# Performance work log

Hardware: AMD Instinct MI355X
Metric: run time of the kernel (lower is better)

Reference implementation:

```python
import jax, jax.numpy as jnp
import numpy as np
from jax import lax

DIM = 256; HEADS = 16; DHEAD = 16; H = 12; W = 26
DS = 4; KOFF = 6; OSCALE = 4.0
SCALE = DHEAD ** -0.5
EPS = 1e-5


def _create_grid(hh, ww, dtype):
    # channel0 = x (width index), channel1 = y (height index); matches torch meshgrid(arange(w), arange(h), indexing='xy')
    gy, gx = jnp.meshgrid(jnp.arange(hh, dtype=dtype), jnp.arange(ww, dtype=dtype), indexing='ij')
    return jnp.stack([gx, gy], axis=0)  # (2, hh, ww)


def _grid_sample_bilinear(img, grid):
    # F.grid_sample, mode='bilinear', padding_mode='zeros', align_corners=False
    # img (B,C,Hi,Wi); grid (B,Ho,Wo,2), grid[...,0]=x-norm, grid[...,1]=y-norm in [-1,1]
    B, C, Hi, Wi = img.shape
    x = ((grid[..., 0] + 1.0) * Wi - 1.0) / 2.0
    y = ((grid[..., 1] + 1.0) * Hi - 1.0) / 2.0
    x0 = jnp.floor(x); y0 = jnp.floor(y)

    def gather(xi, yi):
        valid = ((xi >= 0) & (xi < Wi) & (yi >= 0) & (yi < Hi)).astype(img.dtype)
        xc = jnp.clip(xi, 0, Wi - 1).astype(jnp.int32)
        yc = jnp.clip(yi, 0, Hi - 1).astype(jnp.int32)
        v = jax.vmap(lambda im, yy, xx: im[:, yy, xx])(img, yc, xc)  # (B,C,Ho,Wo)
        return v * valid[:, None]

    wx1 = (x - x0)[:, None]; wx0 = 1.0 - wx1
    wy1 = (y - y0)[:, None]; wy0 = 1.0 - wy1
    return (gather(x0, y0) * wy0 * wx0 + gather(x0 + 1.0, y0) * wy0 * wx1
            + gather(x0, y0 + 1.0) * wy1 * wx0 + gather(x0 + 1.0, y0 + 1.0) * wy1 * wx1)


def _forward(x, q, w_off_dw, b_off_dw, w_off_pw, wk, wv, w_out, b_out,
             cpb_w1, cpb_b1, cpb_w2, cpb_b2, cpb_w3, cpb_b3,
             conv1d_w, conv1d_b, ln_g, ln_b):
    b = x.shape[0]
    # faithful to torch: q.repeat(1,1,h*w).view(bs,1,dim,h,w).squeeze(1) == tile then reshape
    q_map = jnp.tile(q[:, 0, :], (1, H * W)).reshape(b, DIM, H, W)

    # to_offsets: depthwise Conv2d(k=6,s=4,p=1) -> GELU -> 1x1 conv (no bias) -> tanh -> *offset_scale
    t = lax.conv_general_dilated(q_map, w_off_dw, window_strides=(DS, DS),
                                 padding=[(1, 1), (1, 1)], feature_group_count=DIM,
                                 dimension_numbers=('NCHW', 'OIHW', 'NCHW'))
    t = jax.nn.gelu(t + b_off_dw[None, :, None, None], approximate=False)
    off = jnp.tanh(jnp.einsum('oc,bchw->bohw', w_off_pw, t)) * OSCALE  # (b,2,Hk,Wk)
    Hk, Wk = off.shape[-2], off.shape[-1]  # 3, 6

    gkv = _create_grid(Hk, Wk, x.dtype)
    vg0 = gkv[0] + off[:, 0]
    vg1 = gkv[1] + off[:, 1]
    # faithful repo normalize_grid: channel0 / (h-1), channel1 / (w-1)
    n0 = 2.0 * vg0 / max(Hk - 1, 1) - 1.0
    n1 = 2.0 * vg1 / max(Wk - 1, 1) - 1.0
    vgrid_scaled = jnp.stack([n0, n1], axis=-1)  # (b, Hk, Wk, 2)

    kv = _grid_sample_bilinear(x, vgrid_scaled)  # (b, DIM, Hk, Wk)
    k = jnp.einsum('oc,bchw->bohw', wk, kv)
    v = jnp.einsum('oc,bchw->bohw', wv, kv)

    qh = (q_map * SCALE).reshape(b, HEADS, DHEAD, H * W).transpose(0, 1, 3, 2)  # (b,h,i,d)
    kh = k.reshape(b, HEADS, DHEAD, Hk * Wk).transpose(0, 1, 3, 2)              # (b,h,j,d)
    vh = v.reshape(b, HEADS, DHEAD, Hk * Wk).transpose(0, 1, 3, 2)
    sim = jnp.einsum('bhid,bhjd->bhij', qh, kh)  # (b,16,312,18)

    # CPB relative position bias
    gq = _create_grid(H, W, x.dtype)
    gq0 = 2.0 * gq[0] / max(H - 1, 1) - 1.0
    gq1 = 2.0 * gq[1] / max(W - 1, 1) - 1.0
    grid_q = jnp.stack([gq0, gq1], axis=-1).reshape(1, H * W, 2)
    grid_kv = vgrid_scaled.reshape(b, Hk * Wk, 2)
    pos = grid_q[:, :, None, :] - grid_kv[:, None, :, :]       # (b,i,j,2)
    bias = jnp.sign(pos) * jnp.log(jnp.abs(pos) + 1.0)
    bias = jax.nn.relu(bias @ cpb_w1.T + cpb_b1)
    bias = jax.nn.relu(bias @ cpb_w2.T + cpb_b2)
    bias = bias @ cpb_w3.T + cpb_b3                             # (b,i,j,heads)
    sim = sim + bias.transpose(0, 3, 1, 2)

    attn = jax.nn.softmax(sim, axis=-1)  # dropout(0.1) identity in eval
    out = jnp.einsum('bhij,bhjd->bhid', attn, vh)               # (b,h,i,d)
    out = out.transpose(0, 1, 3, 2).reshape(b, DIM, H, W)        # 'b h (x y) d -> b (h d) x y'
    out = jnp.einsum('oc,bchw->bohw', w_out, out) + b_out[None, :, None, None]

    # SpatialCrossAttention tail: view -> permute -> Conv1d(312,1,1) -> residual -> LayerNorm
    tokens = out.reshape(b, DIM, H * W).transpose(0, 2, 1)       # (b,312,256)
    pooled = jnp.einsum('t,btc->bc', conv1d_w, tokens)[:, None, :] + conv1d_b[None, :, None]
    y = pooled + q
    mu = y.mean(-1, keepdims=True)
    var = y.var(-1, keepdims=True)
    return (y - mu) / jnp.sqrt(var + EPS) * ln_g + ln_b          # (b,1,256)


def setup_inputs() -> dict:
    key = jax.random.key(0)
    ks = jax.random.split(key, 16)
    rn = lambda i, shape, s=0.02: jax.random.normal(ks[i], shape, dtype=jnp.float32) * s
    B = 256
    return {
        'x': jax.random.normal(ks[0], (B, DIM, H, W), dtype=jnp.float32),
        'q': jax.random.normal(ks[1], (B, 1, DIM), dtype=jnp.float32),
        'w_off_dw': rn(2, (DIM, 1, KOFF, KOFF), 0.05),
        'b_off_dw': jnp.zeros((DIM,), jnp.float32),
        'w_off_pw': rn(3, (2, DIM), 0.05),
        'wk': rn(4, (DIM, DIM)),
        'wv': rn(5, (DIM, DIM)),
        'w_out': rn(6, (DIM, DIM)),
        'b_out': jnp.zeros((DIM,), jnp.float32),
        'cpb_w1': rn(7, (64, 2), 0.1),
        'cpb_b1': jnp.zeros((64,), jnp.float32),
        'cpb_w2': rn(8, (64, 64), 0.1),
        'cpb_b2': jnp.zeros((64,), jnp.float32),
        'cpb_w3': rn(9, (HEADS, 64), 0.1),
        'cpb_b3': jnp.zeros((HEADS,), jnp.float32),
        'conv1d_w': rn(10, (H * W,), 0.05),
        'conv1d_b': jnp.zeros((1,), jnp.float32),
        'ln_g': jnp.ones((DIM,), jnp.float32),
        'ln_b': jnp.zeros((DIM,), jnp.float32),
    }


def reference(x, q, w_off_dw, b_off_dw, w_off_pw, wk, wv, w_out, b_out,
              cpb_w1, cpb_b1, cpb_w2, cpb_b2, cpb_w3, cpb_b3,
              conv1d_w, conv1d_b, ln_g, ln_b):
    return _forward(x, q, w_off_dw, b_off_dw, w_off_pw, wk, wv, w_out, b_out,
                    cpb_w1, cpb_b1, cpb_w2, cpb_b2, cpb_w3, cpb_b3,
                    conv1d_w, conv1d_b, ln_g, ln_b)
```

## Files before the change

### kernel.cpp

```cpp
#include <hip/hip_runtime.h>
#include <hip/hip_bf16.h>
#include <math.h>


typedef __attribute__((ext_vector_type(8))) short short8;
typedef __attribute__((ext_vector_type(4))) short s4bf;
typedef __attribute__((ext_vector_type(4))) float floatx4;

union U16 { uint4 u; short8 s; };
union U8b { unsigned int u[2]; s4bf s; };

#define MFMA(A, B, C) __builtin_amdgcn_mfma_f32_16x16x32_bf16((A), (B), (C), 0, 0, 0)
#define MFMA16(A, B, C) __builtin_amdgcn_mfma_f32_16x16x16bf16_1k((A), (B), (C), 0, 0, 0)

__device__ __forceinline__ unsigned int f2bf(float f) {
    unsigned int u = __float_as_uint(f);
    u += 0x7fffu + ((u >> 16) & 1u);
    return u >> 16;
}
__device__ __forceinline__ unsigned int pk2(float a, float b) {
    __hip_bfloat162 h = __float22bfloat162_rn(make_float2(a, b));
    union { __hip_bfloat162 h; unsigned int u; } cv; cv.h = h;
    return cv.u;
}
__device__ __forceinline__ float bf2f(unsigned short v) {
    return __uint_as_float((unsigned int)v << 16);
}
__device__ __forceinline__ uint4 pack8(float4 a, float4 b) {
    uint4 r;
    r.x = pk2(a.x, a.y); r.y = pk2(a.z, a.w);
    r.z = pk2(b.x, b.y); r.w = pk2(b.z, b.w);
    return r;
}

__global__ __launch_bounds__(512, 2) void k_all(
    const float* __restrict__ x, const float* __restrict__ q,
    const float* __restrict__ w_dw, const float* __restrict__ b_dw,
    const float* __restrict__ w_pw,
    const float* __restrict__ wk, const float* __restrict__ wv,
    const float* __restrict__ w_out, const float* __restrict__ b_out,
    const float* __restrict__ cw1, const float* __restrict__ cb1,
    const float* __restrict__ cw2, const float* __restrict__ cb2,
    const float* __restrict__ cw3, const float* __restrict__ cb3,
    const float* __restrict__ conv_w, const float* __restrict__ conv_b,
    const float* __restrict__ ln_g, const float* __restrict__ ln_b,
    float* __restrict__ out)
{
    const int b = blockIdx.x, tid = threadIdx.x;
    const int w = tid >> 6, lane = tid & 63;
    const int n = lane & 15, qd = lane >> 4;

    __shared__ float qf_s[256];
    __shared__ unsigned short q_sb[256];
    __shared__ unsigned short v_sb[5120];
    __shared__ float F0[468], F1[216];
    __shared__ unsigned int lutxy[312];
    __shared__ float off_s[36], n0_s[18], n1_s[18];
    __shared__ float sx0[18], sy0[18], swx[18], swy[18];
    __shared__ float b2_s[64], b3_s[16];
    __shared__ __align__(16) float w1p[4][8][8];
    __shared__ float wA_s[288];
    __shared__ __align__(16) float m_s[256];
    __shared__ float pooled_s[256], redb[24];
    __shared__ __align__(16) unsigned char UB[117504];
    float* Sbuf = (float*)UB;
    unsigned short* kvT = (unsigned short*)UB;
    float* qsw = (float*)UB;
    float* t_s = (float*)(UB + 16512);
    unsigned short* k_sb = (unsigned short*)(UB + 16512);
    float* wred = (float*)(UB + 39168);

    if (tid < 256) {
        const float qv = q[b * 256 + tid];
        qf_s[tid] = qv;
        q_sb[tid] = (unsigned short)f2bf(qv * 0.25f);
    }
    for (int u = tid; u < 4128; u += 512) {
        const int r = u / 258, i = u - r * 258;
        qsw[u] = (i < 256) ? q[b * 256 + i] : 0.f;
    }
    if (tid < 312) {
        const int iy = tid / 26;
        lutxy[tid] = (unsigned int)(tid - iy * 26) | ((unsigned int)iy << 16);
    }
    if (tid < 64) b2_s[tid] = cb2[tid];
    if (tid < 16) b3_s[tid] = cb3[tid];
    if (tid >= 64 && tid < 96) {
        const int t2 = tid - 64;
        const int qdi = t2 >> 3, kp = t2 & 7;
        const int kk0 = 2 * kp, kk1 = 2 * kp + 1;
        const int kid0 = (kk0 < 8) ? (qdi * 8 + kk0) : (32 + qdi * 8 + kk0 - 8);
        const int kid1 = (kk1 < 8) ? (qdi * 8 + kk1) : (32 + qdi * 8 + kk1 - 8);
        w1p[qdi][kp][0] = cw1[kid0 * 2];
        w1p[qdi][kp][1] = cw1[kid0 * 2 + 1];
        w1p[qdi][kp][2] = cb1[kid0];
        w1p[qdi][kp][3] = cw1[kid1 * 2];
        w1p[qdi][kp][4] = cw1[kid1 * 2 + 1];
        w1p[qdi][kp][5] = cb1[kid1];
    }
    __syncthreads();

    {
        const int c = tid & 255, g = tid >> 8;
        float wreg[36];
        const float4* wdw4 = (const float4*)w_dw;
        #pragma unroll
        for (int i = 0; i < 9; ++i) {
            const float4 t4 = wdw4[c * 9 + i];
            wreg[i * 4 + 0] = t4.x; wreg[i * 4 + 1] = t4.y;
            wreg[i * 4 + 2] = t4.z; wreg[i * 4 + 3] = t4.w;
        }
        float acc[9];
        const float bv = b_dw[c];
        #pragma unroll
        for (int a = 0; a < 9; ++a) acc[a] = bv;
        const int cb = (c * 56) & 255;
        const int cp = (c & 15) * 258;
        for (int jh = 0; jh < 3; ++jh) {
            for (int kh = 0; kh < 6; ++kh) {
                const int ih = jh * 4 - 1 + kh;
                if (ih < 0 || ih >= 12) continue;
                const int rb = ih * 26;
                #pragma unroll
                for (int jwl = 0; jwl < 3; ++jwl) {
                    const int jw = g * 3 + jwl;
                    #pragma unroll
                    for (int kw = 0; kw < 6; ++kw) {
                        const int iw = jw * 4 - 1 + kw;
                        if (iw < 0 || iw >= 26) continue;
                        acc[jh * 3 + jwl] += wreg[kh * 6 + kw] * qsw[cp + ((cb + rb + iw) & 255)];
                    }
                }
            }
        }
        #pragma unroll
        for (int a = 0; a < 9; ++a) {
            const int jh = a / 3, jwl = a - jh * 3;
            const int p = jh * 6 + g * 3 + jwl;
            const float v = acc[a];
            t_s[p * 256 + c] = 0.5f * v * (1.0f + erff(v * 0.70710678118654752f));
        }
    }
    __syncthreads();

    for (int oi = w; oi < 36; oi += 8) {
        const int o = oi / 18, p = oi - o * 18;
        float s = 0.f;
        for (int c = lane; c < 256; c += 64) s += w_pw[o * 256 + c] * t_s[p * 256 + c];
        for (int d = 32; d > 0; d >>= 1) s += __shfl_down(s, d, 64);
        if (lane == 0) off_s[oi] = 4.0f * tanhf(s);
    }
    __syncthreads();

    if (tid < 18) {
        const int j = tid, jh = j / 6, jw = j - jh * 6;
        const float vg0 = (float)jw + off_s[j];
        const float vg1 = (float)jh + off_s[18 + j];
        const float n0 = 2.0f * vg0 / 2.0f - 1.0f;
        const float n1 = 2.0f * vg1 / 5.0f - 1.0f;
        n0_s[j] = n0; n1_s[j] = n1;
        const float xp = ((n0 + 1.0f) * 26.0f - 1.0f) * 0.5f;
        const float yp = ((n1 + 1.0f) * 12.0f - 1.0f) * 0.5f;
        const float x0 = floorf(xp), y0 = floorf(yp);
        sx0[j] = x0; sy0[j] = y0; swx[j] = xp - x0; swy[j] = yp - y0;
    }
    __syncthreads();

    {
        const int c = tid & 255, g = tid >> 8;
        const float* xb = x + ((size_t)b * 256 + c) * 312;
        for (int jj = 0; jj < 9; ++jj) {
            const int j = g * 9 + jj;
            const int x0 = (int)sx0[j], y0 = (int)sy0[j];
            const int x1 = x0 + 1, y1 = y0 + 1;
            const float wx1 = swx[j], wy1 = swy[j];
            const float wx0 = 1.f - wx1, wy0 = 1.f - wy1;
            const bool xv0 = (x0 >= 0) & (x0 < 26), xv1 = (x1 >= 0) & (x1 < 26);
            const bool yv0 = (y0 >= 0) & (y0 < 12), yv1 = (y1 >= 0) & (y1 < 12);
            const float v00 = (xv0 & yv0) ? xb[y0 * 26 + x0] : 0.f;
            const float v01 = (xv1 & yv0) ? xb[y0 * 26 + x1] : 0.f;
            const float v10 = (xv0 & yv1) ? xb[y1 * 26 + x0] : 0.f;
            const float v11 = (xv1 & yv1) ? xb[y1 * 26 + x1] : 0.f;
            const float val = wy0 * (wx0 * v00 + wx1 * v01) + wy1 * (wx0 * v10 + wx1 * v11);
            kvT[j * 264 + c] = (unsigned short)f2bf(val);
        }
    }
    for (int u = tid; u < 684; u += 512) {
        if (u < 468) {
            const int ixv = u / 18, j = u - ixv * 18;
            const float p0 = (float)ixv * (2.0f / 11.0f) - 1.0f - n0_s[j];
            F0[u] = copysignf(__logf(1.0f + fabsf(p0)), p0);
        } else {
            const int u2 = u - 468;
            const int iyv = u2 / 18, j = u2 - iyv * 18;
            const float p1 = (float)iyv * (2.0f / 25.0f) - 1.0f - n1_s[j];
            F1[u2] = copysignf(__logf(1.0f + fabsf(p1)), p1);
        }
    }
    __syncthreads();

    {
        const int m2 = w & 1, mtb = w >> 1;
        const float4* wm4 = (const float4*)(m2 ? wv : wk);
        floatx4 pa[4][2];
        #pragma unroll
        for (int a = 0; a < 4; ++a) {
            pa[a][0] = (floatx4){0.f, 0.f, 0.f, 0.f};
            pa[a][1] = (floatx4){0.f, 0.f, 0.f, 0.f};
        }
        #pragma unroll 2
        for (int ks = 0; ks < 8; ++ks) {
            U16 b0, b1;
            b0.u = *(const uint4*)(kvT + n * 264 + ks * 32 + qd * 8);
            b1.u = make_uint4(0u, 0u, 0u, 0u);
            if (n < 2) b1.u = *(const uint4*)(kvT + (16 + n) * 264 + ks * 32 + qd * 8);
            #pragma unroll
            for (int mtl = 0; mtl < 4; ++mtl) {
                const int mt = mtb + mtl * 4;
                const int f4i = (mt * 16 + n) * 64 + ks * 8 + qd * 2;
                U16 A; A.u = pack8(wm4[f4i], wm4[f4i + 1]);
                pa[mtl][0] = MFMA(A.s, b0.s, pa[mtl][0]);
                pa[mtl][1] = MFMA(A.s, b1.s, pa[mtl][1]);
            }
        }
        unsigned short* dst = m2 ? v_sb : k_sb;
        #pragma unroll
        for (int mtl = 0; mtl < 4; ++mtl) {
            const int mt = mtb + mtl * 4;
            #pragma unroll
            for (int r = 0; r < 4; ++r) {
                const int o = mt * 16 + qd * 4 + r;
                dst[o * 20 + n] = (unsigned short)f2bf(pa[mtl][0][r]);
                if (n < 2) dst[o * 20 + 16 + n] = (unsigned short)f2bf(pa[mtl][1][r]);
            }
        }
    }
    __syncthreads();

    uint4 W2f[4][2];
    unsigned int W3h[4][2];
    {
        const float4* cw2_4 = (const float4*)cw2;
        #pragma unroll
        for (int mtl = 0; mtl < 4; ++mtl)
            #pragma unroll
            for (int ks = 0; ks < 2; ++ks) {
                const int base = (mtl * 16 + n) * 16 + ks * 8 + qd * 2;
                W2f[mtl][ks] = pack8(cw2_4[base], cw2_4[base + 1]);
            }
        const float4* cw3_4 = (const float4*)cw3;
        #pragma unroll
        for (int kc = 0; kc < 4; ++kc) {
            const float4 v = cw3_4[n * 16 + kc * 4 + qd];
            W3h[kc][0] = pk2(v.x, v.y);
            W3h[kc][1] = pk2(v.z, v.w);
        }
    }

    unsigned int Bk16[2][2][2];
    #pragma unroll
    for (int hh = 0; hh < 2; ++hh)
        #pragma unroll
        for (int jt = 0; jt < 2; ++jt) {
            unsigned int u0 = 0, u1 = 0;
            const int j = jt * 16 + n;
            if (j < 18) {
                const int h = w * 2 + hh;
                const int cb0 = (h * 16 + qd * 4) * 20 + j;
                u0 = (unsigned)k_sb[cb0]      | ((unsigned)k_sb[cb0 + 20] << 16);
                u1 = (unsigned)k_sb[cb0 + 40] | ((unsigned)k_sb[cb0 + 60] << 16);
            }
            Bk16[hh][jt][0] = u0; Bk16[hh][jt][1] = u1;
        }
    int kA[2];
    #pragma unroll
    for (int hh = 0; hh < 2; ++hh)
        kA[hh] = (((w * 2 + hh) * 16 + qd * 4) * 56) & 255;
    __syncthreads();

    float wAcc[18];
    #pragma unroll
    for (int j = 0; j < 18; ++j) wAcc[j] = 0.f;

    auto soft_acc = [&](int chp, const float* Sp) {
        const int il = tid >> 4, h = tid & 15;
        const int CIp = (chp == 9) ? 24 : 32;
        if (il < CIp) {
            const float cwv = conv_w[chp * 32 + il];
            float lv[18];
            const float* row = Sp + (il * 18) * 17 + h;
            #pragma unroll
            for (int j = 0; j < 18; ++j) lv[j] = row[j * 17];
            float mx[9];
            #pragma unroll
            for (int p = 0; p < 9; ++p) mx[p] = fmaxf(lv[2 * p], lv[2 * p + 1]);
            #pragma unroll
            for (int p = 0; p < 4; ++p) mx[p] = fmaxf(mx[p], mx[p + 4]);
            mx[0] = fmaxf(mx[0], mx[2]); mx[1] = fmaxf(mx[1], mx[3]);
            const float m = fmaxf(fmaxf(mx[0], mx[1]), mx[8]);
            float sa = 0.f, sb = 0.f;
            #pragma unroll
            for (int j = 0; j < 18; j += 2) {
                lv[j] = __expf(lv[j] - m);     sa += lv[j];
                lv[j + 1] = __expf(lv[j + 1] - m); sb += lv[j + 1];
            }
            const float wgt = cwv / (sa + sb);
            #pragma unroll
            for (int j = 0; j < 18; ++j) wAcc[j] = fmaf(wgt, lv[j], wAcc[j]);
        }
    };

    for (int t = 0; t < 12; ++t) {
        if (t < 10) {
            float* Sc = Sbuf + (t % 3) * 9792;
            const int ibase = t * 32;
            #pragma unroll
            for (int hh = 0; hh < 2; ++hh) {
                const int h = w * 2 + hh;
                const int ka = kA[hh];
                #pragma unroll
                for (int ig = 0; ig < 2; ++ig) {
                    const int ii = ibase + ig * 16 + n;
                    const unsigned int a0 =
                        (unsigned)q_sb[(ka + ii) & 255] |
                        ((unsigned)q_sb[(ka + 56 + ii) & 255] << 16);
                    const unsigned int a1 =
                        (unsigned)q_sb[(ka + 112 + ii) & 255] |
                        ((unsigned)q_sb[(ka + 168 + ii) & 255] << 16);
                    U8b Af; Af.u[0] = a0; Af.u[1] = a1;
                    #pragma unroll
                    for (int jt = 0; jt < 2; ++jt) {
                        U8b Bf; Bf.u[0] = Bk16[hh][jt][0]; Bf.u[1] = Bk16[hh][jt][1];
                        floatx4 D = {0.f, 0.f, 0.f, 0.f};
                        D = MFMA16(Af.s, Bf.s, D);
                        const int j = jt * 16 + n;
                        if (j < 18) {
                            #pragma unroll
                            for (int r = 0; r < 4; ++r)
                                Sc[((ig * 16 + qd * 4 + r) * 18 + j) * 17 + h] = D[r];
                        }
                    }
                }
            }
        }
        if (t >= 1 && t < 11) {
            const int chm = t - 1;
            float* Sm = Sbuf + (chm % 3) * 9792;
            const int ibase = chm * 32;
            auto mlp1 = [&](int tt) {
                const int ig = (tt >= 18) ? 1 : 0;
                const int j = tt - ig * 18;
                const int i0 = ibase + ig * 16 + n;
                const unsigned int lv2 = lutxy[(i0 < 312) ? i0 : 311];
                const int ix = (int)(lv2 & 0xffffu), iy = (int)(lv2 >> 16);
                const float f0 = F0[ix * 18 + j];
                const float f1 = F1[iy * 18 + j];
                U16 ub0, ub1;
                {
                    unsigned int uu[8];
                    #pragma unroll
                    for (int kp = 0; kp < 8; ++kp) {
                        const float* wp = &w1p[qd][kp][0];
                        const float ha = fmaxf(fmaf(wp[0], f0, fmaf(wp[1], f1, wp[2])), 0.f);
                        const float hb = fmaxf(fmaf(wp[3], f0, fmaf(wp[4], f1, wp[5])), 0.f);
                        uu[kp] = pk2(ha, hb);
                    }
                    ub0.u = make_uint4(uu[0], uu[1], uu[2], uu[3]);
                    ub1.u = make_uint4(uu[4], uu[5], uu[6], uu[7]);
                }
                floatx4 a3a = {0.f, 0.f, 0.f, 0.f};
                floatx4 a3b = {0.f, 0.f, 0.f, 0.f};
                #pragma unroll
                for (int mtl = 0; mtl < 4; ++mtl) {
                    U16 A0, A1; A0.u = W2f[mtl][0]; A1.u = W2f[mtl][1];
                    floatx4 acc = {0.f, 0.f, 0.f, 0.f};
                    acc = MFMA(A0.s, ub0.s, acc);
                    acc = MFMA(A1.s, ub1.s, acc);
                    U8b Bf3, Af3;
                    Bf3.u[0] = pk2(fmaxf(acc[0] + b2_s[mtl*16 + qd*4 + 0], 0.f),
                                   fmaxf(acc[1] + b2_s[mtl*16 + qd*4 + 1], 0.f));
                    Bf3.u[1] = pk2(fmaxf(acc[2] + b2_s[mtl*16 + qd*4 + 2], 0.f),
                                   fmaxf(acc[3] + b2_s[mtl*16 + qd*4 + 3], 0.f));
                    Af3.u[0] = W3h[mtl][0]; Af3.u[1] = W3h[mtl][1];
                    if (mtl & 1) a3b = MFMA16(Af3.s, Bf3.s, a3b);
                    else         a3a = MFMA16(Af3.s, Bf3.s, a3a);
                }
                float* sp = Sm + ((ig * 16 + n) * 18 + j) * 17 + qd * 4;
                #pragma unroll
                for (int r = 0; r < 4; ++r)
                    sp[r] = a3a[r] + a3b[r] + b3_s[qd * 4 + r] + sp[r];
            };
            mlp1(w);
            mlp1(w + 8);
            mlp1(w + 16);
            mlp1(w + 24);
            if (w < 4) mlp1(32 + w);
        }
        if (t >= 2) soft_acc(t - 2, Sbuf + ((t - 2) % 3) * 9792);
        __syncthreads();
    }

    #pragma unroll
    for (int j = 0; j < 18; ++j) wred[tid * 18 + j] = wAcc[j];
    {
        float v = 0.f;
        for (int u = tid; u < 312; u += 512) v += conv_w[u];
        for (int d = 32; d > 0; d >>= 1) v += __shfl_down(v, d, 64);
        if (lane == 0) redb[w] = v;
    }
    __syncthreads();
    for (int u = tid; u < 288; u += 512) {
        const int h = u / 18, j = u - h * 18;
        float s = 0.f;
        #pragma unroll
        for (int sl = 0; sl < 32; ++sl) s += wred[(sl * 16 + h) * 18 + j];
        wA_s[u] = s;
    }
    __syncthreads();

    if (tid < 256) {
        const int hb = (tid >> 4) * 18;
        float acc = 0.f;
        #pragma unroll
        for (int j = 0; j < 18; ++j) acc += wA_s[hb + j] * bf2f(v_sb[tid * 20 + j]);
        m_s[tid] = acc;
    }
    __syncthreads();

    float Ssum = 0.f;
    #pragma unroll
    for (int i = 0; i < 8; ++i) Ssum += redb[i];

    {
        const float4 mm = *(const float4*)(m_s + lane * 4);
        for (int ol = 0; ol < 32; ++ol) {
            const int o = w * 32 + ol;
            const float4 wq = *(const float4*)(w_out + o * 256 + lane * 4);
            float d = wq.x * mm.x + wq.y * mm.y + wq.z * mm.z + wq.w * mm.w;
            for (int dd = 32; dd > 0; dd >>= 1) d += __shfl_down(d, dd, 64);
            if (lane == 0) pooled_s[o] = d;
        }
    }
    __syncthreads();

    if (tid < 256) {
        const float y = pooled_s[tid] + b_out[tid] * Ssum + conv_b[0] + qf_s[tid];
        float s1 = y, s2 = y * y;
        for (int d = 32; d > 0; d >>= 1) { s1 += __shfl_down(s1, d, 64); s2 += __shfl_down(s2, d, 64); }
        if (lane == 0) { redb[16 + w] = s1; redb[20 + w] = s2; }
    }
    __syncthreads();
    if (tid < 256) {
        const float y = pooled_s[tid] + b_out[tid] * Ssum + conv_b[0] + qf_s[tid];
        const float S1 = redb[16] + redb[17] + redb[18] + redb[19];
        const float S2 = redb[20] + redb[21] + redb[22] + redb[23];
        const float mu = S1 * (1.0f / 256.0f);
        const float var = S2 * (1.0f / 256.0f) - mu * mu;
        out[b * 256 + tid] = (y - mu) * rsqrtf(var + 1e-5f) * ln_g[tid] + ln_b[tid];
    }
}

extern "C" void kernel_launch(void* const* d_in, const int* in_sizes, int n_in,
                              void* d_out, int out_size, void* d_ws, size_t ws_size,
                              hipStream_t stream) {
    const float* x       = (const float*)d_in[0];
    const float* q       = (const float*)d_in[1];
    const float* w_dw    = (const float*)d_in[2];
    const float* b_dwp   = (const float*)d_in[3];
    const float* w_pw    = (const float*)d_in[4];
    const float* wk      = (const float*)d_in[5];
    const float* wv      = (const float*)d_in[6];
    const float* w_out   = (const float*)d_in[7];
    const float* b_out   = (const float*)d_in[8];
    const float* cw1     = (const float*)d_in[9];
    const float* cb1     = (const float*)d_in[10];
    const float* cw2     = (const float*)d_in[11];
    const float* cb2     = (const float*)d_in[12];
    const float* cw3     = (const float*)d_in[13];
    const float* cb3     = (const float*)d_in[14];
    const float* conv_w  = (const float*)d_in[15];
    const float* conv_b  = (const float*)d_in[16];
    const float* ln_g    = (const float*)d_in[17];
    const float* ln_b    = (const float*)d_in[18];
    float* out = (float*)d_out;

    k_all<<<256, 512, 0, stream>>>(x, q, w_dw, b_dwp, w_pw, wk, wv, w_out, b_out,
                                   cw1, cb1, cw2, cb2, cw3, cb3,
                                   conv_w, conv_b, ln_g, ln_b, out);
}
```

Baseline: 248.5 us.

## Register-cache CPB layer-1 weights, pair MLP tiles, replicate q buffer per quad

Moves the first CPB MLP layer's weights and biases from shared memory into per-lane registers and processes two (i,j) tiles per call so their MFMA chains interleave. Replicates the bf16 q vector four times in shared memory at a 272-element stride so each lane quad reads its own copy, aiming to cut LDS bank conflicts on the score A-fragment gathers. This adds 48 live floats per thread under launch_bounds(512,2), which risks register spills.

```diff
diff --git a/kernel.cpp b/kernel.cpp
--- a/kernel.cpp
+++ b/kernel.cpp
@@ -51,14 +51,13 @@
     const int n = lane & 15, qd = lane >> 4;
 
     __shared__ float qf_s[256];
-    __shared__ unsigned short q_sb[256];
+    __shared__ unsigned short q_sb4[1088];
     __shared__ unsigned short v_sb[5120];
     __shared__ float F0[468], F1[216];
     __shared__ unsigned int lutxy[312];
     __shared__ float off_s[36], n0_s[18], n1_s[18];
     __shared__ float sx0[18], sy0[18], swx[18], swy[18];
     __shared__ float b2_s[64], b3_s[16];
-    __shared__ __align__(16) float w1p[4][8][8];
     __shared__ float wA_s[288];
     __shared__ __align__(16) float m_s[256];
     __shared__ float pooled_s[256], redb[24];
@@ -73,7 +72,9 @@
     if (tid < 256) {
         const float qv = q[b * 256 + tid];
         qf_s[tid] = qv;
-        q_sb[tid] = (unsigned short)f2bf(qv * 0.25f);
+        const unsigned short qb = (unsigned short)f2bf(qv * 0.25f);
+        q_sb4[tid] = qb; q_sb4[272 + tid] = qb;
+        q_sb4[544 + tid] = qb; q_sb4[816 + tid] = qb;
     }
     for (int u = tid; u < 4128; u += 512) {
         const int r = u / 258, i = u - r * 258;
@@ -85,19 +86,6 @@
     }
     if (tid < 64) b2_s[tid] = cb2[tid];
     if (tid < 16) b3_s[tid] = cb3[tid];
-    if (tid >= 64 && tid < 96) {
-        const int t2 = tid - 64;
-        const int qdi = t2 >> 3, kp = t2 & 7;
-        const int kk0 = 2 * kp, kk1 = 2 * kp + 1;
-        const int kid0 = (kk0 < 8) ? (qdi * 8 + kk0) : (32 + qdi * 8 + kk0 - 8);
-        const int kid1 = (kk1 < 8) ? (qdi * 8 + kk1) : (32 + qdi * 8 + kk1 - 8);
-        w1p[qdi][kp][0] = cw1[kid0 * 2];
-        w1p[qdi][kp][1] = cw1[kid0 * 2 + 1];
-        w1p[qdi][kp][2] = cb1[kid0];
-        w1p[qdi][kp][3] = cw1[kid1 * 2];
-        w1p[qdi][kp][4] = cw1[kid1 * 2 + 1];
-        w1p[qdi][kp][5] = cb1[kid1];
-    }
     __syncthreads();
 
     {
@@ -256,6 +244,12 @@
             W3h[kc][1] = pk2(v.z, v.w);
         }
     }
+    float W1a[16], W1b[16], B1r[16];
+    #pragma unroll
+    for (int kk = 0; kk < 16; ++kk) {
+        const int kid = (kk < 8) ? (qd * 8 + kk) : (32 + qd * 8 + kk - 8);
+        W1a[kk] = cw1[kid * 2]; W1b[kk] = cw1[kid * 2 + 1]; B1r[kk] = cb1[kid];
+    }
 
     unsigned int Bk16[2][2][2];
     #pragma unroll
@@ -314,6 +308,7 @@
         if (t < 10) {
             float* Sc = Sbuf + (t % 3) * 9792;
             const int ibase = t * 32;
+            const unsigned short* qsb = q_sb4 + qd * 272;
             #pragma unroll
             for (int hh = 0; hh < 2; ++hh) {
                 const int h = w * 2 + hh;
@@ -322,11 +317,11 @@
                 for (int ig = 0; ig < 2; ++ig) {
                     const int ii = ibase + ig * 16 + n;
                     const unsigned int a0 =
-                        (unsigned)q_sb[(ka + ii) & 255] |
-                        ((unsigned)q_sb[(ka + 56 + ii) & 255] << 16);
+                        (unsigned)qsb[(ka + ii) & 255] |
+                        ((unsigned)qsb[(ka + 56 + ii) & 255] << 16);
                     const unsigned int a1 =
-                        (unsigned)q_sb[(ka + 112 + ii) & 255] |
-                        ((unsigned)q_sb[(ka + 168 + ii) & 255] << 16);
+                        (unsigned)qsb[(ka + 112 + ii) & 255] |
+                        ((unsigned)qsb[(ka + 168 + ii) & 255] << 16);
                     U8b Af; Af.u[0] = a0; Af.u[1] = a1;
                     #pragma unroll
                     for (int jt = 0; jt < 2; ++jt) {
@@ -347,54 +342,71 @@
             const int chm = t - 1;
             float* Sm = Sbuf + (chm % 3) * 9792;
             const int ibase = chm * 32;
-            auto mlp1 = [&](int tt) {
-                const int ig = (tt >= 18) ? 1 : 0;
-                const int j = tt - ig * 18;
-                const int i0 = ibase + ig * 16 + n;
-                const unsigned int lv2 = lutxy[(i0 < 312) ? i0 : 311];
-                const int ix = (int)(lv2 & 0xffffu), iy = (int)(lv2 >> 16);
-                const float f0 = F0[ix * 18 + j];
-                const float f1 = F1[iy * 18 + j];
-                U16 ub0, ub1;
-                {
+            auto mlp2 = [&](int tA, int tB, bool two) {
+                int igv[2], jv[2];
+                float f0v[2], f1v[2];
+                #pragma unroll
+                for (int u = 0; u < 2; ++u) {
+                    const int tt = u ? tB : tA;
+                    const int ig = (tt >= 18) ? 1 : 0;
+                    const int j = tt - ig * 18;
+                    igv[u] = ig; jv[u] = j;
+                    const int i0 = ibase + ig * 16 + n;
+                    const unsigned int lv2 = lutxy[(i0 < 312) ? i0 : 311];
+                    const int ix = (int)(lv2 & 0xffffu), iy = (int)(lv2 >> 16);
+                    f0v[u] = F0[ix * 18 + j];
+                    f1v[u] = F1[iy * 18 + j];
+                }
+                U16 ub0[2], ub1[2];
+                #pragma unroll
+                for (int u = 0; u < 2; ++u) {
                     unsigned int uu[8];
                     #pragma unroll
                     for (int kp = 0; kp < 8; ++kp) {
-                        const float* wp = &w1p[qd][kp][0];
-                        const float ha = fmaxf(fmaf(wp[0], f0, fmaf(wp[1], f1, wp[2])), 0.f);
-                        const float hb = fmaxf(fmaf(wp[3], f0, fmaf(wp[4], f1, wp[5])), 0.f);
+                        const float ha = fmaxf(fmaf(W1a[2*kp],   f0v[u], fmaf(W1b[2*kp],   f1v[u], B1r[2*kp])),   0.f);
+                        const float hb = fmaxf(fmaf(W1a[2*kp+1], f0v[u], fmaf(W1b[2*kp+1], f1v[u], B1r[2*kp+1])), 0.f);
                         uu[kp] = pk2(ha, hb);
                     }
-                    ub0.u = make_uint4(uu[0], uu[1], uu[2], uu[3]);
-                    ub1.u = make_uint4(uu[4], uu[5], uu[6], uu[7]);
-                }
-                floatx4 a3a = {0.f, 0.f, 0.f, 0.f};
-                floatx4 a3b = {0.f, 0.f, 0.f, 0.f};
+                    ub0[u].u = make_uint4(uu[0], uu[1], uu[2], uu[3]);
+                    ub1[u].u = make_uint4(uu[4], uu[5], uu[6], uu[7]);
+                }
+                floatx4 a3a[2], a3b[2];
+                #pragma unroll
+                for (int u = 0; u < 2; ++u) {
+                    a3a[u] = (floatx4){0.f, 0.f, 0.f, 0.f};
+                    a3b[u] = (floatx4){0.f, 0.f, 0.f, 0.f};
+                }
                 #pragma unroll
                 for (int mtl = 0; mtl < 4; ++mtl) {
                     U16 A0, A1; A0.u = W2f[mtl][0]; A1.u = W2f[mtl][1];
-                    floatx4 acc = {0.f, 0.f, 0.f, 0.f};
-                    acc = MFMA(A0.s, ub0.s, acc);
-                    acc = MFMA(A1.s, ub1.s, acc);
-                    U8b Bf3, Af3;
-                    Bf3.u[0] = pk2(fmaxf(acc[0] + b2_s[mtl*16 + qd*4 + 0], 0.f),
-                                   fmaxf(acc[1] + b2_s[mtl*16 + qd*4 + 1], 0.f));
-                    Bf3.u[1] = pk2(fmaxf(acc[2] + b2_s[mtl*16 + qd*4 + 2], 0.f),
-                                   fmaxf(acc[3] + b2_s[mtl*16 + qd*4 + 3], 0.f));
-                    Af3.u[0] = W3h[mtl][0]; Af3.u[1] = W3h[mtl][1];
-                    if (mtl & 1) a3b = MFMA16(Af3.s, Bf3.s, a3b);
-                    else         a3a = MFMA16(Af3.s, Bf3.s, a3a);
-                }
-                float* sp = Sm + ((ig * 16 + n) * 18 + j) * 17 + qd * 4;
-                #pragma unroll
-                for (int r = 0; r < 4; ++r)
-                    sp[r] = a3a[r] + a3b[r] + b3_s[qd * 4 + r] + sp[r];
+                    #pragma unroll
+                    for (int u = 0; u < 2; ++u) {
+                        if (u == 1 && !two) break;
+                        floatx4 acc = {0.f, 0.f, 0.f, 0.f};
+                        acc = MFMA(A0.s, ub0[u].s, acc);
+                        acc = MFMA(A1.s, ub1[u].s, acc);
+                        U8b Bf3, Af3;
+                        Bf3.u[0] = pk2(fmaxf(acc[0] + b2_s[mtl*16 + qd*4 + 0], 0.f),
+                                       fmaxf(acc[1] + b2_s[mtl*16 + qd*4 + 1], 0.f));
+                        Bf3.u[1] = pk2(fmaxf(acc[2] + b2_s[mtl*16 + qd*4 + 2], 0.f),
+                                       fmaxf(acc[3] + b2_s[mtl*16 + qd*4 + 3], 0.f));
+                        Af3.u[0] = W3h[mtl][0]; Af3.u[1] = W3h[mtl][1];
+                        if (mtl & 1) a3b[u] = MFMA16(Af3.s, Bf3.s, a3b[u]);
+                        else         a3a[u] = MFMA16(Af3.s, Bf3.s, a3a[u]);
+                    }
+                }
+                #pragma unroll
+                for (int u = 0; u < 2; ++u) {
+                    if (u == 1 && !two) break;
+                    float* sp = Sm + ((igv[u] * 16 + n) * 18 + jv[u]) * 17 + qd * 4;
+                    #pragma unroll
+                    for (int r = 0; r < 4; ++r)
+                        sp[r] = a3a[u][r] + a3b[u][r] + b3_s[qd * 4 + r] + sp[r];
+                }
             };
-            mlp1(w);
-            mlp1(w + 8);
-            mlp1(w + 16);
-            mlp1(w + 24);
-            if (w < 4) mlp1(32 + w);
+            mlp2(w, w + 8, true);
+            mlp2(w + 16, w + 24, true);
+            if (w < 4) mlp2(32 + w, 32 + w, false);
         }
         if (t >= 2) soft_acc(t - 2, Sbuf + ((t - 2) % 3) * 9792);
         __syncthreads();
```

Measured after the change: 249.9 us. No clear change (+0.6%).
